# Kernel optimization log

Measured on AMD Instinct MI355X. Metric: run time of the kernel, lower is better.

Reference implementation:

```python
import jax, jax.numpy as jnp
import numpy as np

B, T, D = 2, 2048, 2048
N, K, H = 16, 4, 128  # query heads, kv heads, head dim
G = N // K            # GQA groups
MIN_TS, MAX_TS = 1.0, 10000.0


def rope(x, positions):
    # x: [B, S, heads, H], positions: [B, S] int
    half = H // 2
    fraction = 2.0 * jnp.arange(half, dtype=jnp.float32) / H
    timescale = MIN_TS * (MAX_TS / MIN_TS) ** fraction            # [half]
    sinusoid = positions.astype(jnp.float32)[:, :, None, None] / timescale  # [B,S,1,half]
    sin, cos = jnp.sin(sinusoid), jnp.cos(sinusoid)
    x1, x2 = x[..., :half], x[..., half:]
    return jnp.concatenate([x1 * cos - x2 * sin, x2 * cos + x1 * sin], axis=-1)


def setup_inputs() -> dict:
    key = jax.random.key(0)
    ks = jax.random.split(key, 6)
    pos = jnp.tile(jnp.arange(T, dtype=jnp.int32)[None, :], (B, 1))
    return {
        "Xq": jax.random.normal(ks[0], (B, T, D), jnp.float32),
        "Xkv": jax.random.normal(ks[1], (B, T, D), jnp.float32),
        "q_positions": pos,
        "kv_positions": pos,
        "Wq": jax.random.normal(ks[2], (D, N, H), jnp.float32) * 0.02,
        "Wk": jax.random.normal(ks[3], (D, K, H), jnp.float32) * 0.02,
        "Wv": jax.random.normal(ks[4], (D, K, H), jnp.float32) * 0.02,
        "Wo": jax.random.normal(ks[5], (N, H, D), jnp.float32) * 0.02,
    }


def reference(Xq, Xkv, q_positions, kv_positions, Wq, Wk, Wv, Wo):
    # QKV projections (tensordot over embed dim), fp32
    q = jnp.einsum("btd,dnh->btnh", Xq, Wq)          # [B,T,N,H]
    k = jnp.einsum("bsd,dkh->bskh", Xkv, Wk)         # [B,S,K,H]
    v = jnp.einsum("bsd,dkh->bskh", Xkv, Wv)
    # inline RoPE on q and k
    q = rope(q, q_positions)
    k = rope(k, kv_positions)
    # GQA: group query heads over kv heads -> [B,K,G,T,H]
    qg = q.transpose(0, 2, 1, 3).reshape(B, K, G, T, H)
    kt = k.transpose(0, 2, 1, 3)                      # [B,K,S,H]
    vt = v.transpose(0, 2, 1, 3)
    scale = 1.0 / jnp.sqrt(jnp.float32(H))
    scores = jnp.einsum("bkgth,bksh->bkgts", qg, kt) * scale
    # causal mask (self-attn, no explicit mask, T>1)
    causal = jnp.tril(jnp.ones((T, T), dtype=bool))
    scores = jnp.where(causal[None, None, None], scores, jnp.finfo(scores.dtype).min)
    probs = jax.nn.softmax(scores, axis=-1)
    attn = jnp.einsum("bkgts,bksh->bkgth", probs, vt)  # [B,K,G,T,H]
    attn = attn.reshape(B, N, T, H).transpose(0, 2, 1, 3)  # [B,T,N,H]
    out = jnp.einsum("btnh,nhd->btd", attn, Wo)
    return out
```

## Files before the change

kernel.cpp:

```cpp
#include <hip/hip_runtime.h>
#include <hip/hip_bf16.h>
#include <cstdint>
#include <cstddef>

#define Bdim 2
#define Tdim 2048
#define Ddim 2048
#define NHq  16
#define NKV  4
#define HD   128
#define SCALE 0.08838834764831845f
#define QPRESCALE (0.08838834764831845f * 1.4426950408889634f)
#define NEG_INF (-3.0e38f)
#define DEFER_THR 11.5f

typedef unsigned short u16;
typedef unsigned int   u32;
typedef __bf16 bf16x8 __attribute__((ext_vector_type(8)));
typedef float  f32x4  __attribute__((ext_vector_type(4)));

__device__ __forceinline__ u16 f2bf(float f) {
    unsigned int u = __float_as_uint(f);
    u += 0x7FFFu + ((u >> 16) & 1u);
    return (u16)(u >> 16);
}
__device__ __forceinline__ u16 f2bfn(float f) {
    __bf16 h = (__bf16)f;
    return __builtin_bit_cast(u16, h);
}
__device__ __forceinline__ float bf2f(u16 s) {
    return __uint_as_float(((unsigned int)s) << 16);
}

#if __has_builtin(__builtin_amdgcn_permlane16_swap) && __has_builtin(__builtin_amdgcn_permlane32_swap)
#define HAVE_PERMLANE_SWAP 1
#endif

__device__ __forceinline__ float quad_reduce_max(float v) {
#ifdef HAVE_PERMLANE_SWAP
    auto r = __builtin_amdgcn_permlane16_swap(__float_as_uint(v), __float_as_uint(v), false, false);
    float m = fmaxf(__uint_as_float(r[0]), __uint_as_float(r[1]));
    auto r2 = __builtin_amdgcn_permlane32_swap(__float_as_uint(m), __float_as_uint(m), false, false);
    return fmaxf(__uint_as_float(r2[0]), __uint_as_float(r2[1]));
#else
    v = fmaxf(v, __shfl_xor(v, 16));
    return fmaxf(v, __shfl_xor(v, 32));
#endif
}
__device__ __forceinline__ float quad_reduce_sum(float v) {
#ifdef HAVE_PERMLANE_SWAP
    auto r = __builtin_amdgcn_permlane16_swap(__float_as_uint(v), __float_as_uint(v), false, false);
    float s = __uint_as_float(r[0]) + __uint_as_float(r[1]);
    auto r2 = __builtin_amdgcn_permlane32_swap(__float_as_uint(s), __float_as_uint(s), false, false);
    return __uint_as_float(r2[0]) + __uint_as_float(r2[1]);
#else
    v += __shfl_xor(v, 16);
    return v + __shfl_xor(v, 32);
#endif
}

__device__ __forceinline__ float tree_max16(const float (&s)[16]) {
    float a0 = fmaxf(s[0], s[1]),  a1 = fmaxf(s[2], s[3]);
    float a2 = fmaxf(s[4], s[5]),  a3 = fmaxf(s[6], s[7]);
    float a4 = fmaxf(s[8], s[9]),  a5 = fmaxf(s[10], s[11]);
    float a6 = fmaxf(s[12], s[13]), a7 = fmaxf(s[14], s[15]);
    float b0 = fmaxf(a0, a1), b1 = fmaxf(a2, a3);
    float b2 = fmaxf(a4, a5), b3 = fmaxf(a6, a7);
    return fmaxf(fmaxf(b0, b1), fmaxf(b2, b3));
}
__device__ __forceinline__ float tree_sum16(const float (&s)[16]) {
    float a0 = s[0] + s[1],  a1 = s[2] + s[3];
    float a2 = s[4] + s[5],  a3 = s[6] + s[7];
    float a4 = s[8] + s[9],  a5 = s[10] + s[11];
    float a6 = s[12] + s[13], a7 = s[14] + s[15];
    float b0 = a0 + a1, b1 = a2 + a3, b2 = a4 + a5, b3 = a6 + a7;
    return (b0 + b1) + (b2 + b3);
}

typedef __attribute__((address_space(1))) const u32 gbl_u32;
typedef __attribute__((address_space(3))) u32 lds_u32;
__device__ __forceinline__ void gload16(const void* g, void* l) {
    __builtin_amdgcn_global_load_lds((gbl_u32*)(uintptr_t)g, (lds_u32*)(uintptr_t)l, 16, 0, 0);
}

__global__ __launch_bounds__(256) void cvt_x(const float* __restrict__ Xq,
                                             const float* __restrict__ Xkv,
                                             u16* __restrict__ oq,
                                             u16* __restrict__ okv)
{
    const size_t NE = (size_t)4096 * 2048 / 8;
    size_t idx = (size_t)blockIdx.x * 256 + threadIdx.x;
    const float* src; u16* dst; size_t off;
    if (idx < NE) { src = Xq;  dst = oq;  off = idx * 8; }
    else          { src = Xkv; dst = okv; off = (idx - NE) * 8; }
    float4 a = *(const float4*)&src[off];
    float4 b = *(const float4*)&src[off + 4];
    ushort4 r0, r1;
    r0.x = f2bf(a.x); r0.y = f2bf(a.y); r0.z = f2bf(a.z); r0.w = f2bf(a.w);
    r1.x = f2bf(b.x); r1.y = f2bf(b.y); r1.z = f2bf(b.z); r1.w = f2bf(b.w);
    *(ushort4*)&dst[off] = r0;
    *(ushort4*)&dst[off + 4] = r1;
}

__global__ __launch_bounds__(256) void cvt_w_t(const float* __restrict__ src,
                                               u16* __restrict__ dst, int R, int C)
{
    __shared__ u16 t[64][72];
    const int r0 = blockIdx.y * 64, c0 = blockIdx.x * 64;
    const int tid = threadIdx.x;
    const int tr = tid >> 4, tc4 = (tid & 15) * 4;
#pragma unroll
    for (int p = 0; p < 4; p++) {
        int r = p * 16 + tr;
        float4 v = *(const float4*)&src[(size_t)(r0 + r) * C + c0 + tc4];
        t[tc4 + 0][r] = f2bf(v.x);
        t[tc4 + 1][r] = f2bf(v.y);
        t[tc4 + 2][r] = f2bf(v.z);
        t[tc4 + 3][r] = f2bf(v.w);
    }
    __syncthreads();
#pragma unroll
    for (int p = 0; p < 4; p++) {
        int cc = p * 16 + tr;
        ushort4 w = *(const ushort4*)&t[cc][tc4];
        *(ushort4*)&dst[(size_t)(c0 + cc) * R + r0 + tc4] = w;
    }
}

__device__ __forceinline__ void bf16_gemm_mainloop(const u16* __restrict__ A,
                                                   const u16* __restrict__ Bt,
                                                   int m0, int n0,
                                                   u16 (&As)[128 * 32],
                                                   u16 (&Bs)[128 * 32],
                                                   f32x4 (&acc)[4][4])
{
    const int tid = threadIdx.x;
    const int wv = tid >> 6, lane = tid & 63;
    const int l15 = lane & 15, quad = lane >> 4;
    const int wr = wv >> 1, wc = wv & 1;

#pragma unroll
    for (int mt = 0; mt < 4; mt++)
#pragma unroll
        for (int nt = 0; nt < 4; nt++) acc[mt][nt] = (f32x4){0.f, 0.f, 0.f, 0.f};

    for (int k0 = 0; k0 < 2048; k0 += 32) {
        __syncthreads();
#pragma unroll
        for (int j = 0; j < 2; j++) {
            int c = wv * 128 + j * 64 + lane;
            const u16* ga = A + (size_t)(m0 + (c >> 2)) * 2048 + k0 + (c & 3) * 8;
            gload16(ga, &As[(wv * 128 + j * 64) * 8]);
            const u16* gb = Bt + (size_t)(n0 + (c >> 2)) * 2048 + k0 + (c & 3) * 8;
            gload16(gb, &Bs[(wv * 128 + j * 64) * 8]);
        }
        __syncthreads();

        bf16x8 af[4], bfr[4];
#pragma unroll
        for (int mt = 0; mt < 4; mt++)
            af[mt] = *(const bf16x8*)&As[(wr * 64 + mt * 16 + l15) * 32 + quad * 8];
#pragma unroll
        for (int nt = 0; nt < 4; nt++)
            bfr[nt] = *(const bf16x8*)&Bs[(wc * 64 + nt * 16 + l15) * 32 + quad * 8];
#pragma unroll
        for (int mt = 0; mt < 4; mt++)
#pragma unroll
            for (int nt = 0; nt < 4; nt++)
                acc[mt][nt] = __builtin_amdgcn_mfma_f32_16x16x32_bf16(af[mt], bfr[nt], acc[mt][nt], 0, 0, 0);
    }
}

__global__ __launch_bounds__(256) void qkv_gemm_bf(const u16* __restrict__ Xq,
                                                   const u16* __restrict__ Xkv,
                                                   const u16* __restrict__ Wqt,
                                                   const u16* __restrict__ Wkt,
                                                   const u16* __restrict__ Wvt,
                                                   u16* __restrict__ qraw,
                                                   u16* __restrict__ kraw,
                                                   u16* __restrict__ vt)
{
    __shared__ __align__(16) u16 As[128 * 32];
    __shared__ __align__(16) u16 Bs[128 * 32];
    f32x4 acc[4][4];
    const int bx = blockIdx.x, m0 = blockIdx.y * 128;
    const u16 *A, *Bt; int n0;
    if (bx < 16)      { A = Xq;  Bt = Wqt; n0 = bx * 128; }
    else if (bx < 20) { A = Xkv; Bt = Wkt; n0 = (bx - 16) * 128; }
    else              { A = Xkv; Bt = Wvt; n0 = (bx - 20) * 128; }
    bf16_gemm_mainloop(A, Bt, m0, n0, As, Bs, acc);

    const int tid = threadIdx.x;
    const int wv = tid >> 6, lane = tid & 63;
    const int l15 = lane & 15, quad = lane >> 4;
    const int wr = wv >> 1, wc = wv & 1;

    if (bx < 20) {
        u16* out; int ldw;
        if (bx < 16) { out = qraw; ldw = 2048; }
        else         { out = kraw; ldw = 512; }
#pragma unroll
        for (int mt = 0; mt < 4; mt++)
#pragma unroll
            for (int nt = 0; nt < 4; nt++) {
                int col = n0 + wc * 64 + nt * 16 + l15;
                int r = m0 + wr * 64 + mt * 16 + quad * 4;
#pragma unroll
                for (int reg = 0; reg < 4; reg++)
                    out[(size_t)(r + reg) * ldw + col] = f2bf(acc[mt][nt][reg]);
            }
    } else {
        const int b = m0 >> 11, tb = m0 & 2047;
#pragma unroll
        for (int mt = 0; mt < 4; mt++)
#pragma unroll
            for (int nt = 0; nt < 4; nt++) {
                int col = n0 + wc * 64 + nt * 16 + l15;
                int tloc = tb + wr * 64 + mt * 16 + quad * 4;
                ushort4 w4;
                w4.x = f2bf(acc[mt][nt][0]);
                w4.y = f2bf(acc[mt][nt][1]);
                w4.z = f2bf(acc[mt][nt][2]);
                w4.w = f2bf(acc[mt][nt][3]);
                *(ushort4*)&vt[((size_t)b * 512 + col) * 2048 + tloc] = w4;
            }
    }
}

__global__ __launch_bounds__(256) void oproj_gemm_bf(const u16* __restrict__ attnb,
                                                     const u16* __restrict__ Wot,
                                                     float* __restrict__ out)
{
    __shared__ __align__(16) u16 As[128 * 32];
    __shared__ __align__(16) u16 Bs[128 * 32];
    f32x4 acc[4][4];
    const int m0 = blockIdx.y * 128, n0 = blockIdx.x * 128;
    bf16_gemm_mainloop(attnb, Wot, m0, n0, As, Bs, acc);
    const int tid = threadIdx.x;
    const int wv = tid >> 6, lane = tid & 63;
    const int l15 = lane & 15, quad = lane >> 4;
    const int wr = wv >> 1, wc = wv & 1;
#pragma unroll
    for (int mt = 0; mt < 4; mt++)
#pragma unroll
        for (int nt = 0; nt < 4; nt++) {
            int col = n0 + wc * 64 + nt * 16 + l15;
            int r = m0 + wr * 64 + mt * 16 + quad * 4;
#pragma unroll
            for (int reg = 0; reg < 4; reg++)
                out[(size_t)(r + reg) * 2048 + col] = acc[mt][nt][reg];
        }
}

__global__ __launch_bounds__(256) void rope_bf(u16* __restrict__ q,
                                               u16* __restrict__ k,
                                               const int* __restrict__ qpos,
                                               const int* __restrict__ kvpos)
{
    const int qTh = Bdim * Tdim * NHq * 16;
    int idx = blockIdx.x * 256 + threadIdx.x;
    u16* base; int h4; int pos; float osc;
    if (idx < qTh) {
        int rn = idx >> 4; h4 = (idx & 15) * 4;
        pos = qpos[rn >> 4];
        base = q + (size_t)rn * HD;
        osc = QPRESCALE;
    } else {
        int j = idx - qTh;
        int rn = j >> 4; h4 = (j & 15) * 4;
        pos = kvpos[rn >> 2];
        base = k + (size_t)rn * HD;
        osc = 1.0f;
    }
    ushort4 a = *(const ushort4*)&base[h4];
    ushort4 bvec = *(const ushort4*)&base[h4 + 64];
    u16 av[4] = {a.x, a.y, a.z, a.w};
    u16 bv[4] = {bvec.x, bvec.y, bvec.z, bvec.w};
#pragma unroll
    for (int j = 0; j < 4; j++) {
        float inv_ts = expf(-(float)(h4 + j) * 0.14391156831f);
        float ang = (float)pos * inv_ts;
        float s, c;
        sincosf(ang, &s, &c);
        s *= osc; c *= osc;
        float x1 = bf2f(av[j]), x2 = bf2f(bv[j]);
        av[j] = f2bf(x1 * c - x2 * s);
        bv[j] = f2bf(x2 * c + x1 * s);
    }
    ushort4 ra, rb;
    ra.x = av[0]; ra.y = av[1]; ra.z = av[2]; ra.w = av[3];
    rb.x = bv[0]; rb.y = bv[1]; rb.z = bv[2]; rb.w = bv[3];
    *(ushort4*)&base[h4] = ra;
    *(ushort4*)&base[h4 + 64] = rb;
}

__global__ __launch_bounds__(512, 4) void flash_attn_v5(const u16* __restrict__ qh,
                                                        const u16* __restrict__ kh,
                                                        const u16* __restrict__ vtg,
                                                        u16* __restrict__ attnb)
{
    __shared__ __align__(16) u16 Ks[2][64 * 128];
    __shared__ __align__(16) u16 Vt[2][128 * 64];
    __shared__ __align__(16) u16 Ps[128 * 64];

    const int yy = blockIdx.y;
    const int qt = (yy < 8) ? (15 - yy) : (yy - 8);
    const int bh = blockIdx.x;
    const int b = bh >> 4, n = bh & 15, kvh = n >> 2;
    const int q0 = qt * 128;
    const int tid = threadIdx.x;
    const int wv = tid >> 6, lane = tid & 63;
    const int l15 = lane & 15, quad = lane >> 4;

    const size_t kbase = (size_t)(b * Tdim) * 512 + kvh * 128;
    const size_t vbase = ((size_t)(b * 512 + kvh * 128)) * 2048;
    const int nT = 2 * qt + 2;

    auto stage = [&](int t, int buf) {
        const int s0s = t * 64;
#pragma unroll
        for (int c = 0; c < 2; c++) {
            int j = c * 512 + tid;
            int s = j >> 4;
            int c8 = (j & 15) ^ (s & 7);
            gload16(kh + kbase + (size_t)(s0s + s) * 512 + c8 * 8,
                    &Ks[buf][(c * 512 + wv * 64) * 8]);
            int h = j >> 3;
            int sb = (j & 7) ^ (h & 7);
            gload16(vtg + vbase + (size_t)h * 2048 + s0s + sb * 8,
                    &Vt[buf][(c * 512 + wv * 64) * 8]);
        }
    };

    stage(0, 0);

    bf16x8 qfrag[4];
    {
        const size_t qbase = ((size_t)(b * Tdim + q0 + wv * 16)) * 2048 + n * 128;
#pragma unroll
        for (int kt = 0; kt < 4; kt++)
            qfrag[kt] = *(const bf16x8*)(qh + qbase + (size_t)l15 * 2048
                                          + kt * 32 + quad * 8);
    }

    f32x4 Oacc[8];
#pragma unroll
    for (int ht = 0; ht < 8; ht++) Oacc[ht] = (f32x4){0.f, 0.f, 0.f, 0.f};
    float mrow = NEG_INF;
    float lrow = 0.f;

    __syncthreads();

    int cur = 0;
    for (int t = 0; t < nT; t++) {
        const int s0 = t * 64;

        if (t + 1 < nT) stage(t + 1, cur ^ 1);

        f32x4 S[4];
#pragma unroll
        for (int nt = 0; nt < 4; nt++) S[nt] = (f32x4){0.f, 0.f, 0.f, 0.f};
#pragma unroll
        for (int kt = 0; kt < 4; kt++) {
            bf16x8 kf[4];
#pragma unroll
            for (int nt = 0; nt < 4; nt++) {
                int s = nt * 16 + l15;
                int cb = (kt * 4 + quad) ^ (s & 7);
                kf[nt] = *(const bf16x8*)&Ks[cur][s * 128 + cb * 8];
            }
#pragma unroll
            for (int nt = 0; nt < 4; nt++)
                S[nt] = __builtin_amdgcn_mfma_f32_16x16x32_bf16(kf[nt], qfrag[kt], S[nt], 0, 0, 0);
        }

        const bool domask = (t >= nT - 2);
        const int m_l = wv * 16 + l15;
        const int mg = q0 + m_l;
        float sv[16];
#pragma unroll
        for (int nt = 0; nt < 4; nt++)
#pragma unroll
            for (int r = 0; r < 4; r++) {
                float vv = S[nt][r];
                if (domask) {
                    int sg = s0 + nt * 16 + quad * 4 + r;
                    if (sg > mg) vv = NEG_INF;
                }
                sv[nt * 4 + r] = vv;
            }
        float mx = quad_reduce_max(tree_max16(sv));
        const bool skip = __all(mx <= mrow + DEFER_THR);
        const float mNew = skip ? mrow : fmaxf(mrow, mx);
#pragma unroll
        for (int i = 0; i < 16; i++)
            sv[i] = __builtin_amdgcn_exp2f(sv[i] - mNew);
#pragma unroll
        for (int nt = 0; nt < 4; nt++) {
            int sb = nt * 2 + (quad >> 1);
            int cb = sb ^ (m_l & 7);
            ushort4 pw;
            pw.x = f2bfn(sv[nt * 4 + 0]);
            pw.y = f2bfn(sv[nt * 4 + 1]);
            pw.z = f2bfn(sv[nt * 4 + 2]);
            pw.w = f2bfn(sv[nt * 4 + 3]);
            *(ushort4*)&Ps[m_l * 64 + cb * 8 + (quad & 1) * 4] = pw;
        }
        {
            float ps = quad_reduce_sum(tree_sum16(sv));
            if (skip) {
                lrow += ps;
            } else {
                float alpha = __builtin_amdgcn_exp2f(mrow - mNew);
                mrow = mNew;
                lrow = lrow * alpha + ps;
                float a0 = __shfl(alpha, quad * 4 + 0);
                float a1 = __shfl(alpha, quad * 4 + 1);
                float a2 = __shfl(alpha, quad * 4 + 2);
                float a3 = __shfl(alpha, quad * 4 + 3);
#pragma unroll
                for (int ht = 0; ht < 8; ht++) {
                    Oacc[ht][0] *= a0;
                    Oacc[ht][1] *= a1;
                    Oacc[ht][2] *= a2;
                    Oacc[ht][3] *= a3;
                }
            }
        }

#pragma unroll
        for (int k2 = 0; k2 < 2; k2++) {
            int cbp = (k2 * 4 + quad) ^ (m_l & 7);
            bf16x8 pf = *(const bf16x8*)&Ps[m_l * 64 + cbp * 8];
#pragma unroll
            for (int ht = 0; ht < 8; ht++) {
                int h = ht * 16 + l15;
                int cb = (k2 * 4 + quad) ^ (h & 7);
                bf16x8 vf = *(const bf16x8*)&Vt[cur][h * 64 + cb * 8];
                Oacc[ht] = __builtin_amdgcn_mfma_f32_16x16x32_bf16(pf, vf, Oacc[ht], 0, 0, 0);
            }
        }

        __syncthreads();
        cur ^= 1;
    }

    {
        f32x4 inv;
#pragma unroll
        for (int r = 0; r < 4; r++)
            inv[r] = 1.0f / __shfl(lrow, quad * 4 + r);
        int mg0 = q0 + wv * 16 + quad * 4;
        u16* dst0 = attnb + ((size_t)(b * Tdim + mg0)) * 2048 + n * 128 + l15;
#pragma unroll
        for (int ht = 0; ht < 8; ht++) {
#pragma unroll
            for (int r = 0; r < 4; r++)
                dst0[(size_t)r * 2048 + ht * 16] = f2bfn(Oacc[ht][r] * inv[r]);
        }
    }
}

extern "C" void kernel_launch(void* const* d_in, const int* in_sizes, int n_in,
                              void* d_out, int out_size, void* d_ws, size_t ws_size,
                              hipStream_t stream) {
    const float* Xq    = (const float*)d_in[0];
    const float* Xkv   = (const float*)d_in[1];
    const int*   qpos  = (const int*)d_in[2];
    const int*   kvpos = (const int*)d_in[3];
    const float* Wq    = (const float*)d_in[4];
    const float* Wk    = (const float*)d_in[5];
    const float* Wv    = (const float*)d_in[6];
    const float* Wo    = (const float*)d_in[7];
    float* out = (float*)d_out;

    char* w = (char*)d_ws;
    u16* xq_bf = (u16*)(w);
    u16* xkv_bf= (u16*)(w + (16u << 20));
    u16* qraw  = (u16*)(w + (32u << 20));
    u16* kraw  = (u16*)(w + (48u << 20));
    u16* vt    = (u16*)(w + (52u << 20));
    u16* wq_t  = (u16*)(w + (56u << 20));
    u16* wk_t  = (u16*)(w + (64u << 20));
    u16* wv_t  = (u16*)(w + (66u << 20));
    u16* wo_t  = (u16*)(w + (68u << 20));
    u16* attnb = (u16*)(w);

    cvt_x<<<8192, 256, 0, stream>>>(Xq, Xkv, xq_bf, xkv_bf);
    cvt_w_t<<<dim3(32, 32), 256, 0, stream>>>(Wq, wq_t, 2048, 2048);
    cvt_w_t<<<dim3(8, 32),  256, 0, stream>>>(Wk, wk_t, 2048, 512);
    cvt_w_t<<<dim3(8, 32),  256, 0, stream>>>(Wv, wv_t, 2048, 512);
    cvt_w_t<<<dim3(32, 32), 256, 0, stream>>>(Wo, wo_t, 2048, 2048);
    qkv_gemm_bf<<<dim3(24, 32), 256, 0, stream>>>(xq_bf, xkv_bf, wq_t, wk_t, wv_t,
                                                  qraw, kraw, vt);
    rope_bf<<<5120, 256, 0, stream>>>(qraw, kraw, qpos, kvpos);
    flash_attn_v5<<<dim3(32, 16), 512, 0, stream>>>(qraw, kraw, vt, attnb);
    oproj_gemm_bf<<<dim3(16, 32), 256, 0, stream>>>(attnb, wo_t, out);
}
```

Baseline: 377.5 us.

## Double-buffer GEMM shared-memory tiles and swizzle block order across XCDs

The bf16 GEMM mainloop now uses two LDS buffers and issues the next k-tile's global-to-LDS loads before the MFMAs on the current tile, leaving one barrier per iteration instead of two. This is meant to overlap global load latency with compute. Both the QKV and output projection kernels also remap block IDs with a stride-8 swizzle, presumably so neighbouring tiles share L2 on the same XCD. LDS use per block doubles, which may lower occupancy.

```diff
diff --git a/kernel.cpp b/kernel.cpp
--- a/kernel.cpp
+++ b/kernel.cpp
@@ -130,8 +130,8 @@
 __device__ __forceinline__ void bf16_gemm_mainloop(const u16* __restrict__ A,
                                                    const u16* __restrict__ Bt,
                                                    int m0, int n0,
-                                                   u16 (&As)[128 * 32],
-                                                   u16 (&Bs)[128 * 32],
+                                                   u16 (&As)[2][128 * 32],
+                                                   u16 (&Bs)[2][128 * 32],
                                                    f32x4 (&acc)[4][4])
 {
     const int tid = threadIdx.x;
@@ -144,30 +144,39 @@
 #pragma unroll
         for (int nt = 0; nt < 4; nt++) acc[mt][nt] = (f32x4){0.f, 0.f, 0.f, 0.f};
 
-    for (int k0 = 0; k0 < 2048; k0 += 32) {
-        __syncthreads();
+    auto stage = [&](int k0, int buf) {
 #pragma unroll
         for (int j = 0; j < 2; j++) {
             int c = wv * 128 + j * 64 + lane;
             const u16* ga = A + (size_t)(m0 + (c >> 2)) * 2048 + k0 + (c & 3) * 8;
-            gload16(ga, &As[(wv * 128 + j * 64) * 8]);
+            gload16(ga, &As[buf][(wv * 128 + j * 64) * 8]);
             const u16* gb = Bt + (size_t)(n0 + (c >> 2)) * 2048 + k0 + (c & 3) * 8;
-            gload16(gb, &Bs[(wv * 128 + j * 64) * 8]);
-        }
-        __syncthreads();
+            gload16(gb, &Bs[buf][(wv * 128 + j * 64) * 8]);
+        }
+    };
+
+    stage(0, 0);
+    __syncthreads();
+
+    int cur = 0;
+    for (int k0 = 0; k0 < 2048; k0 += 32) {
+        if (k0 + 32 < 2048) stage(k0 + 32, cur ^ 1);
 
         bf16x8 af[4], bfr[4];
 #pragma unroll
         for (int mt = 0; mt < 4; mt++)
-            af[mt] = *(const bf16x8*)&As[(wr * 64 + mt * 16 + l15) * 32 + quad * 8];
+            af[mt] = *(const bf16x8*)&As[cur][(wr * 64 + mt * 16 + l15) * 32 + quad * 8];
 #pragma unroll
         for (int nt = 0; nt < 4; nt++)
-            bfr[nt] = *(const bf16x8*)&Bs[(wc * 64 + nt * 16 + l15) * 32 + quad * 8];
+            bfr[nt] = *(const bf16x8*)&Bs[cur][(wc * 64 + nt * 16 + l15) * 32 + quad * 8];
 #pragma unroll
         for (int mt = 0; mt < 4; mt++)
 #pragma unroll
             for (int nt = 0; nt < 4; nt++)
                 acc[mt][nt] = __builtin_amdgcn_mfma_f32_16x16x32_bf16(af[mt], bfr[nt], acc[mt][nt], 0, 0, 0);
+
+        __syncthreads();
+        cur ^= 1;
     }
 }
 
@@ -180,10 +189,13 @@
                                                    u16* __restrict__ kraw,
                                                    u16* __restrict__ vt)
 {
-    __shared__ __align__(16) u16 As[128 * 32];
-    __shared__ __align__(16) u16 Bs[128 * 32];
+    __shared__ __align__(16) u16 As[2][128 * 32];
+    __shared__ __align__(16) u16 Bs[2][128 * 32];
     f32x4 acc[4][4];
-    const int bx = blockIdx.x, m0 = blockIdx.y * 128;
+    const int bid0 = (int)blockIdx.x + 24 * (int)blockIdx.y;
+    const int swz  = (bid0 & 7) * 96 + (bid0 >> 3);
+    const int bx   = swz % 24;
+    const int m0   = (swz / 24) * 128;
     const u16 *A, *Bt; int n0;
     if (bx < 16)      { A = Xq;  Bt = Wqt; n0 = bx * 128; }
     else if (bx < 20) { A = Xkv; Bt = Wkt; n0 = (bx - 16) * 128; }
@@ -231,10 +243,13 @@
                                                      const u16* __restrict__ Wot,
                                                      float* __restrict__ out)
 {
-    __shared__ __align__(16) u16 As[128 * 32];
-    __shared__ __align__(16) u16 Bs[128 * 32];
+    __shared__ __align__(16) u16 As[2][128 * 32];
+    __shared__ __align__(16) u16 Bs[2][128 * 32];
     f32x4 acc[4][4];
-    const int m0 = blockIdx.y * 128, n0 = blockIdx.x * 128;
+    const int bid0 = (int)blockIdx.x + 16 * (int)blockIdx.y;
+    const int swz  = (bid0 & 7) * 64 + (bid0 >> 3);
+    const int n0   = (swz & 15) * 128;
+    const int m0   = (swz >> 4) * 128;
     bf16_gemm_mainloop(attnb, Wot, m0, n0, As, Bs, acc);
     const int tid = threadIdx.x;
     const int wv = tid >> 6, lane = tid & 63;
```

Measured after the change: 353.7 us. 6.3% less time.

## Rewrite QKV and output-projection GEMMs as 256x256 multi-stage pipelined MFMA kernels

Applied to the files above, without the earlier changes.

Replaces the 128x128, 256-thread, single-buffered bf16 GEMM mainloop with a 256x256-tile, 512-thread kernel. It double-buffers LDS with K split into halves and uses explicit vmcnt waits, raw barriers and setprio so async global-to-LDS loads overlap MFMA work. It also XOR-swizzles LDS columns to avoid bank conflicts and remaps block IDs for L2 locality. Larger tiles raise data reuse per block, but they cut the grid to 192 and 128 blocks on a 256-CU part, which risks underfilling the device. The hand-written waitcnt schedule is fragile.

```diff
diff --git a/kernel.cpp b/kernel.cpp
--- a/kernel.cpp
+++ b/kernel.cpp
@@ -82,6 +82,12 @@
 __device__ __forceinline__ void gload16(const void* g, void* l) {
     __builtin_amdgcn_global_load_lds((gbl_u32*)(uintptr_t)g, (lds_u32*)(uintptr_t)l, 16, 0, 0);
 }
+
+#define VM8 asm volatile("s_waitcnt vmcnt(8)" ::: "memory")
+#define VM4 asm volatile("s_waitcnt vmcnt(4)" ::: "memory")
+#define VM0 asm volatile("s_waitcnt vmcnt(0)" ::: "memory")
+#define VMNONE ((void)0)
+#define BARRIER do { asm volatile("" ::: "memory"); __builtin_amdgcn_s_barrier(); asm volatile("" ::: "memory"); } while (0)
 
 __global__ __launch_bounds__(256) void cvt_x(const float* __restrict__ Xq,
                                              const float* __restrict__ Xkv,
@@ -127,128 +133,193 @@
     }
 }
 
-__device__ __forceinline__ void bf16_gemm_mainloop(const u16* __restrict__ A,
-                                                   const u16* __restrict__ Bt,
-                                                   int m0, int n0,
-                                                   u16 (&As)[128 * 32],
-                                                   u16 (&Bs)[128 * 32],
-                                                   f32x4 (&acc)[4][4])
+#define GPH(c, ks, mh, STAGE, VMW) do {                                        \
+    bf16x8 Af[4];                                                              \
+    _Pragma("unroll")                                                          \
+    for (int mf = 0; mf < 4; mf++)                                             \
+        Af[mf] = *(const bf16x8*)&Ab[c][ks][(arow + (mh) * 64 + mf * 16) * 32 + cxs]; \
+    if ((mh) == 0) {                                                           \
+        _Pragma("unroll")                                                      \
+        for (int nf = 0; nf < 4; nf++)                                         \
+            Bf[nf] = *(const bf16x8*)&Bb[c][ks][(brow + nf * 16) * 32 + cxs];  \
+    }                                                                          \
+    STAGE;                                                                     \
+    BARRIER;                                                                   \
+    asm volatile("s_waitcnt lgkmcnt(0)" ::: "memory");                         \
+    __builtin_amdgcn_s_setprio(1);                                             \
+    _Pragma("unroll")                                                          \
+    for (int mf = 0; mf < 4; mf++)                                             \
+        _Pragma("unroll")                                                      \
+        for (int nf = 0; nf < 4; nf++)                                         \
+            acc[(mh) * 4 + mf][nf] = __builtin_amdgcn_mfma_f32_16x16x32_bf16(  \
+                Af[mf], Bf[nf], acc[(mh) * 4 + mf][nf], 0, 0, 0);              \
+    __builtin_amdgcn_s_setprio(0);                                             \
+    VMW;                                                                       \
+    BARRIER;                                                                   \
+} while (0)
+
+__device__ __forceinline__ void gemm8_mainloop(const u16* __restrict__ A,
+                                               const u16* __restrict__ Bt,
+                                               int m0, int n0,
+                                               u16 (&Ab)[2][2][256 * 32],
+                                               u16 (&Bb)[2][2][256 * 32],
+                                               f32x4 (&acc)[8][4])
 {
     const int tid = threadIdx.x;
     const int wv = tid >> 6, lane = tid & 63;
     const int l15 = lane & 15, quad = lane >> 4;
-    const int wr = wv >> 1, wc = wv & 1;
-
-#pragma unroll
-    for (int mt = 0; mt < 4; mt++)
-#pragma unroll
-        for (int nt = 0; nt < 4; nt++) acc[mt][nt] = (f32x4){0.f, 0.f, 0.f, 0.f};
-
-    for (int k0 = 0; k0 < 2048; k0 += 32) {
-        __syncthreads();
+    const int wr = wv >> 2, wc = wv & 3;
+
+#pragma unroll
+    for (int mf = 0; mf < 8; mf++)
+#pragma unroll
+        for (int nf = 0; nf < 4; nf++) acc[mf][nf] = (f32x4){0.f, 0.f, 0.f, 0.f};
+
+    auto stageA = [&](int kt, int kh, int c) {
 #pragma unroll
         for (int j = 0; j < 2; j++) {
-            int c = wv * 128 + j * 64 + lane;
-            const u16* ga = A + (size_t)(m0 + (c >> 2)) * 2048 + k0 + (c & 3) * 8;
-            gload16(ga, &As[(wv * 128 + j * 64) * 8]);
-            const u16* gb = Bt + (size_t)(n0 + (c >> 2)) * 2048 + k0 + (c & 3) * 8;
-            gload16(gb, &Bs[(wv * 128 + j * 64) * 8]);
-        }
-        __syncthreads();
-
-        bf16x8 af[4], bfr[4];
-#pragma unroll
-        for (int mt = 0; mt < 4; mt++)
-            af[mt] = *(const bf16x8*)&As[(wr * 64 + mt * 16 + l15) * 32 + quad * 8];
-#pragma unroll
-        for (int nt = 0; nt < 4; nt++)
-            bfr[nt] = *(const bf16x8*)&Bs[(wc * 64 + nt * 16 + l15) * 32 + quad * 8];
-#pragma unroll
-        for (int mt = 0; mt < 4; mt++)
-#pragma unroll
-            for (int nt = 0; nt < 4; nt++)
-                acc[mt][nt] = __builtin_amdgcn_mfma_f32_16x16x32_bf16(af[mt], bfr[nt], acc[mt][nt], 0, 0, 0);
-    }
-}
-
-__global__ __launch_bounds__(256) void qkv_gemm_bf(const u16* __restrict__ Xq,
-                                                   const u16* __restrict__ Xkv,
-                                                   const u16* __restrict__ Wqt,
-                                                   const u16* __restrict__ Wkt,
-                                                   const u16* __restrict__ Wvt,
-                                                   u16* __restrict__ qraw,
-                                                   u16* __restrict__ kraw,
-                                                   u16* __restrict__ vt)
-{
-    __shared__ __align__(16) u16 As[128 * 32];
-    __shared__ __align__(16) u16 Bs[128 * 32];
-    f32x4 acc[4][4];
-    const int bx = blockIdx.x, m0 = blockIdx.y * 128;
-    const u16 *A, *Bt; int n0;
-    if (bx < 16)      { A = Xq;  Bt = Wqt; n0 = bx * 128; }
-    else if (bx < 20) { A = Xkv; Bt = Wkt; n0 = (bx - 16) * 128; }
-    else              { A = Xkv; Bt = Wvt; n0 = (bx - 20) * 128; }
-    bf16_gemm_mainloop(A, Bt, m0, n0, As, Bs, acc);
+            int q = j * 512 + tid;
+            int r = q >> 2;
+            int c4 = (q & 3) ^ (r & 3);
+            gload16(A + (size_t)(m0 + r) * 2048 + kt * 64 + kh * 32 + c4 * 8,
+                    &Ab[c][kh][q * 8]);
+        }
+    };
+    auto stageB = [&](int kt, int kh, int c) {
+#pragma unroll
+        for (int j = 0; j < 2; j++) {
+            int q = j * 512 + tid;
+            int r = q >> 2;
+            int c4 = (q & 3) ^ (r & 3);
+            gload16(Bt + (size_t)(n0 + r) * 2048 + kt * 64 + kh * 32 + c4 * 8,
+                    &Bb[c][kh][q * 8]);
+        }
+    };
+
+    const int arow = wr * 128 + l15;
+    const int brow = wc * 64 + l15;
+    const int cxs  = (quad ^ (l15 & 3)) * 8;
+
+    stageA(0, 0, 0); stageB(0, 0, 0);
+    stageA(0, 1, 0); stageB(0, 1, 0);
+    stageA(1, 0, 1); stageB(1, 0, 1);
+    VM8;
+    BARRIER;
+
+    bf16x8 Bf[4];
+    for (int it = 0; it < 15; it++) {
+        const int t0 = 2 * it, t1 = 2 * it + 1;
+        GPH(0, 0, 0, { stageA(t1, 1, 1); },     VMNONE);
+        GPH(0, 0, 1, { stageB(t1, 1, 1); },     VM8);
+        GPH(0, 1, 0, { stageA(t0 + 2, 0, 0); }, VMNONE);
+        GPH(0, 1, 1, { stageB(t0 + 2, 0, 0); }, VM8);
+        GPH(1, 0, 0, { stageA(t0 + 2, 1, 0); }, VMNONE);
+        GPH(1, 0, 1, { stageB(t0 + 2, 1, 0); }, VM8);
+        GPH(1, 1, 0, { stageA(t1 + 2, 0, 1); }, VMNONE);
+        GPH(1, 1, 1, { stageB(t1 + 2, 0, 1); }, VM8);
+    }
+    GPH(0, 0, 0, { stageA(31, 1, 1); }, VMNONE);
+    GPH(0, 0, 1, { stageB(31, 1, 1); }, VM8);
+    GPH(0, 1, 0, VMNONE, VMNONE);
+    GPH(0, 1, 1, VMNONE, VM4);
+    GPH(1, 0, 0, VMNONE, VMNONE);
+    GPH(1, 0, 1, VMNONE, VM0);
+    GPH(1, 1, 0, VMNONE, VMNONE);
+    GPH(1, 1, 1, VMNONE, VMNONE);
+}
+
+__global__ __launch_bounds__(512, 2) void qkv_gemm8(const u16* __restrict__ Xq,
+                                                    const u16* __restrict__ Xkv,
+                                                    const u16* __restrict__ Wqt,
+                                                    const u16* __restrict__ Wkt,
+                                                    const u16* __restrict__ Wvt,
+                                                    u16* __restrict__ qraw,
+                                                    u16* __restrict__ kraw,
+                                                    u16* __restrict__ vt)
+{
+    __shared__ __align__(16) u16 Ab[2][2][256 * 32];
+    __shared__ __align__(16) u16 Bb[2][2][256 * 32];
+    f32x4 acc[8][4];
+
+    const int bid0 = (int)blockIdx.x + 12 * (int)blockIdx.y;
+    const int swz  = (bid0 & 7) * 24 + (bid0 >> 3);
+    const int cx   = swz % 12;
+    const int m0   = (swz / 12) * 256;
+
+    const u16 *A, *Bt; int nb;
+    if (cx < 8)       { A = Xq;  Bt = Wqt; nb = cx * 256; }
+    else if (cx < 10) { A = Xkv; Bt = Wkt; nb = (cx - 8) * 256; }
+    else              { A = Xkv; Bt = Wvt; nb = (cx - 10) * 256; }
+
+    gemm8_mainloop(A, Bt, m0, nb, Ab, Bb, acc);
 
     const int tid = threadIdx.x;
     const int wv = tid >> 6, lane = tid & 63;
     const int l15 = lane & 15, quad = lane >> 4;
-    const int wr = wv >> 1, wc = wv & 1;
-
-    if (bx < 20) {
+    const int wr = wv >> 2, wc = wv & 3;
+    const int row0 = m0 + wr * 128;
+
+    if (cx < 10) {
         u16* out; int ldw;
-        if (bx < 16) { out = qraw; ldw = 2048; }
-        else         { out = kraw; ldw = 512; }
-#pragma unroll
-        for (int mt = 0; mt < 4; mt++)
-#pragma unroll
-            for (int nt = 0; nt < 4; nt++) {
-                int col = n0 + wc * 64 + nt * 16 + l15;
-                int r = m0 + wr * 64 + mt * 16 + quad * 4;
+        if (cx < 8) { out = qraw; ldw = 2048; }
+        else        { out = kraw; ldw = 512; }
+#pragma unroll
+        for (int mf = 0; mf < 8; mf++)
+#pragma unroll
+            for (int nf = 0; nf < 4; nf++) {
+                int col = nb + wc * 64 + nf * 16 + l15;
+                int r = row0 + mf * 16 + quad * 4;
 #pragma unroll
                 for (int reg = 0; reg < 4; reg++)
-                    out[(size_t)(r + reg) * ldw + col] = f2bf(acc[mt][nt][reg]);
+                    out[(size_t)(r + reg) * ldw + col] = f2bf(acc[mf][nf][reg]);
             }
     } else {
-        const int b = m0 >> 11, tb = m0 & 2047;
-#pragma unroll
-        for (int mt = 0; mt < 4; mt++)
-#pragma unroll
-            for (int nt = 0; nt < 4; nt++) {
-                int col = n0 + wc * 64 + nt * 16 + l15;
-                int tloc = tb + wr * 64 + mt * 16 + quad * 4;
+        const int b = m0 >> 11;
+#pragma unroll
+        for (int mf = 0; mf < 8; mf++)
+#pragma unroll
+            for (int nf = 0; nf < 4; nf++) {
+                int col = nb + wc * 64 + nf * 16 + l15;
+                int tloc = ((row0 & 2047) + mf * 16 + quad * 4);
                 ushort4 w4;
-                w4.x = f2bf(acc[mt][nt][0]);
-                w4.y = f2bf(acc[mt][nt][1]);
-                w4.z = f2bf(acc[mt][nt][2]);
-                w4.w = f2bf(acc[mt][nt][3]);
-                *(ushort4*)&vt[((size_t)b * 512 + col) * 2048 + tloc] = w4;
+                w4.x = f2bf(acc[mf][nf][0]);
+                w4.y = f2bf(acc[mf][nf][1]);
+                w4.z = f2bf(acc[mf][nf][2]);
+                w4.w = f2bf(acc[mf][nf][3]);
+                *(ushort4*)&vt[((size_t)(b * 512 + col)) * 2048 + tloc] = w4;
             }
     }
 }
 
-__global__ __launch_bounds__(256) void oproj_gemm_bf(const u16* __restrict__ attnb,
-                                                     const u16* __restrict__ Wot,
-                                                     float* __restrict__ out)
-{
-    __shared__ __align__(16) u16 As[128 * 32];
-    __shared__ __align__(16) u16 Bs[128 * 32];
-    f32x4 acc[4][4];
-    const int m0 = blockIdx.y * 128, n0 = blockIdx.x * 128;
-    bf16_gemm_mainloop(attnb, Wot, m0, n0, As, Bs, acc);
+__global__ __launch_bounds__(512, 2) void oproj_gemm8(const u16* __restrict__ attnb,
+                                                      const u16* __restrict__ Wot,
+                                                      float* __restrict__ out)
+{
+    __shared__ __align__(16) u16 Ab[2][2][256 * 32];
+    __shared__ __align__(16) u16 Bb[2][2][256 * 32];
+    f32x4 acc[8][4];
+
+    const int bid0 = (int)blockIdx.x + 8 * (int)blockIdx.y;
+    const int swz  = (bid0 & 7) * 16 + (bid0 >> 3);
+    const int n0   = (swz % 8) * 256;
+    const int m0   = (swz / 8) * 256;
+
+    gemm8_mainloop(attnb, Wot, m0, n0, Ab, Bb, acc);
+
     const int tid = threadIdx.x;
     const int wv = tid >> 6, lane = tid & 63;
     const int l15 = lane & 15, quad = lane >> 4;
-    const int wr = wv >> 1, wc = wv & 1;
-#pragma unroll
-    for (int mt = 0; mt < 4; mt++)
-#pragma unroll
-        for (int nt = 0; nt < 4; nt++) {
-            int col = n0 + wc * 64 + nt * 16 + l15;
-            int r = m0 + wr * 64 + mt * 16 + quad * 4;
+    const int wr = wv >> 2, wc = wv & 3;
+    const int row0 = m0 + wr * 128;
+#pragma unroll
+    for (int mf = 0; mf < 8; mf++)
+#pragma unroll
+        for (int nf = 0; nf < 4; nf++) {
+            int col = n0 + wc * 64 + nf * 16 + l15;
+            int r = row0 + mf * 16 + quad * 4;
 #pragma unroll
             for (int reg = 0; reg < 4; reg++)
-                out[(size_t)(r + reg) * 2048 + col] = acc[mt][nt][reg];
+                out[(size_t)(r + reg) * 2048 + col] = acc[mf][nf][reg];
         }
 }
 
@@ -491,9 +562,9 @@
     cvt_w_t<<<dim3(8, 32),  256, 0, stream>>>(Wk, wk_t, 2048, 512);
     cvt_w_t<<<dim3(8, 32),  256, 0, stream>>>(Wv, wv_t, 2048, 512);
     cvt_w_t<<<dim3(32, 32), 256, 0, stream>>>(Wo, wo_t, 2048, 2048);
-    qkv_gemm_bf<<<dim3(24, 32), 256, 0, stream>>>(xq_bf, xkv_bf, wq_t, wk_t, wv_t,
-                                                  qraw, kraw, vt);
+    qkv_gemm8<<<dim3(12, 16), 512, 0, stream>>>(xq_bf, xkv_bf, wq_t, wk_t, wv_t,
+                                                qraw, kraw, vt);
     rope_bf<<<5120, 256, 0, stream>>>(qraw, kraw, qpos, kvpos);
     flash_attn_v5<<<dim3(32, 16), 512, 0, stream>>>(qraw, kraw, vt, attnb);
-    oproj_gemm_bf<<<dim3(16, 32), 256, 0, stream>>>(attnb, wo_t, out);
-}
+    oproj_gemm8<<<dim3(8, 16), 512, 0, stream>>>(attnb, wo_t, out);
+}
```

Measured after the change: 349.1 us. -7.5%, faster.
